# Kernel tuning notes

Measured on AMD Instinct MI355X. Metric: run time of the kernel, lower is better.

## Reference

```python
import jax, jax.numpy as jnp
import numpy as np

B, S, D, H = 2, 2048, 1024, 16
HD = D // H                 # head_dim = 64
BLOCK = 16                  # _DEFAULT_BLOCK_SIZE
NB = S // BLOCK             # max_blocks_per_seq = 128
WINDOW = 512
NEG = jnp.float32(-1e30)


def setup_inputs() -> dict:
    key = jax.random.key(0)
    ks = jax.random.split(key, 5)
    x = jax.random.normal(ks[0], (B, S, D), jnp.float32)
    scale = D ** -0.5
    wq = jax.random.normal(ks[1], (D, D), jnp.float32) * scale
    wk = jax.random.normal(ks[2], (D, D), jnp.float32) * scale
    wv = jax.random.normal(ks[3], (D, D), jnp.float32) * scale
    wo = jax.random.normal(ks[4], (D, D), jnp.float32) * scale
    # sequential paged layout (matches the module's synthesized-cache fallback)
    block_tables = jnp.arange(B * NB, dtype=jnp.int32).reshape(B, NB)
    slot_mapping = jnp.arange(B * S, dtype=jnp.int32)
    context_lens = jnp.full((B,), S, dtype=jnp.int32)
    return {"x": x, "wq": wq, "wk": wk, "wv": wv, "wo": wo,
            "block_tables": block_tables, "slot_mapping": slot_mapping,
            "context_lens": context_lens, "window_size": WINDOW}


def reference(x, wq, wk, wv, wo, block_tables, slot_mapping, context_lens, window_size):
    b, s, d = x.shape
    # Q/K/V projections (nn.Linear, bias=False: y = x @ W^T)
    q = (x @ wq.T).reshape(b, s, H, HD)
    k = (x @ wk.T).reshape(b, s, H, HD)
    v = (x @ wv.T).reshape(b, s, H, HD)

    # ---- memopt_C.write_cache: scatter K/V into the physical slot pool ----
    num_slots = b * s
    key_cache = jnp.zeros((num_slots, H, HD), x.dtype).at[slot_mapping].set(k.reshape(-1, H, HD))
    value_cache = jnp.zeros((num_slots, H, HD), x.dtype).at[slot_mapping].set(v.reshape(-1, H, HD))

    # ---- dynamic_sparse_attention: read KV through block_tables ----
    t = jnp.arange(s)
    # physical slot of logical token t of sequence b: block_tables[b, t//BLOCK]*BLOCK + t%BLOCK
    slots = block_tables[:, t // BLOCK].astype(jnp.int32) * BLOCK + (t % BLOCK)[None, :].astype(jnp.int32)  # [B,S]
    kc = key_cache[slots]    # [B,S,H,HD]
    vc = value_cache[slots]  # [B,S,H,HD]

    scores = jnp.einsum('bqhd,bkhd->bhqk', q, kc) * (HD ** -0.5)  # [B,H,S,S]
    qpos = t[:, None]
    kpos = t[None, :]
    # causal + window-limited visibility (window_size tokens of history)
    vis = (kpos <= qpos) & (qpos - kpos < window_size)            # [S,S]
    ctx = t[None, :] < context_lens[:, None]                       # [B,S]
    mask = vis[None, None, :, :] & ctx[:, None, None, :]
    scores = jnp.where(mask, scores, NEG)
    attn = jax.nn.softmax(scores, axis=-1)
    out = jnp.einsum('bhqk,bkhd->bqhd', attn, vc).reshape(b, s, d)
    return out @ wo.T
```

## Files before the change

kernel.cpp:

```cpp
#include <hip/hip_runtime.h>

typedef __attribute__((ext_vector_type(4))) float  f32x4;
typedef __attribute__((ext_vector_type(8))) short  bf16x8;

typedef __attribute__((address_space(3))) void lds_void_t;
typedef __attribute__((address_space(1))) void g_void_t;

#define S_LEN  2048
#define DMODEL 1024
#define NHEAD  16
#define HDIM   64
#define NBLK   128
#define BATCH  2
#define KT     64
#define VP     72

__device__ __forceinline__ short f2bf(float f) {
  union { float f; unsigned u; } v; v.f = f;
  unsigned r = v.u + 0x7fffu + ((v.u >> 16) & 1u);
  return (short)(r >> 16);
}

__global__ __launch_bounds__(256) void cvt_all_kernel(
    const float* __restrict__ x,  const float* __restrict__ wq,
    const float* __restrict__ wk, const float* __restrict__ wv,
    const float* __restrict__ wo,
    short* __restrict__ xb,  short* __restrict__ wqb,
    short* __restrict__ wkb, short* __restrict__ wvb,
    short* __restrict__ wob) {
  const long i = ((long)blockIdx.x * 256 + threadIdx.x) * 8;
  const float* s; short* d; long off;
  if (i < 4194304L)      { s = x;  d = xb;  off = i; }
  else if (i < 5242880L) { s = wq; d = wqb; off = i - 4194304L; }
  else if (i < 6291456L) { s = wk; d = wkb; off = i - 5242880L; }
  else if (i < 7340032L) { s = wv; d = wvb; off = i - 6291456L; }
  else                   { s = wo; d = wob; off = i - 7340032L; }
  f32x4 a = *(const f32x4*)(s + off);
  f32x4 b = *(const f32x4*)(s + off + 4);
  bf16x8 o;
  o[0]=f2bf(a[0]); o[1]=f2bf(a[1]); o[2]=f2bf(a[2]); o[3]=f2bf(a[3]);
  o[4]=f2bf(b[0]); o[5]=f2bf(b[1]); o[6]=f2bf(b[2]); o[7]=f2bf(b[3]);
  *(bf16x8*)(d + off) = o;
}

__global__ __launch_bounds__(512, 2) void gemm8_kernel(
    const short* __restrict__ A,
    const short* __restrict__ W0, const short* __restrict__ W1, const short* __restrict__ W2,
    const int* __restrict__ slot_map,
    short* __restrict__ qbuf, short* __restrict__ kcache, short* __restrict__ vcache)
{
  extern __shared__ short smem[];

  const int m0 = blockIdx.x * 256;
  const int n0 = blockIdx.y * 192;
  const short* Ag = A + (size_t)m0 * DMODEL;

  const int tid  = threadIdx.x;
  const int wave = tid >> 6, lane = tid & 63;
  const int l15 = lane & 15, lg = lane >> 4;
  const int wr = wave >> 2, wc = wave & 3;
  const int swz = l15 & 7;

  short* const A0s = smem;
  short* const B0s = smem + 16384;
  short* const A1s = smem + 28672;
  short* const B1s = smem + 45056;

  f32x4 acc[8][3];
#pragma unroll
  for (int m = 0; m < 8; m++)
#pragma unroll
    for (int n = 0; n < 3; n++) acc[m][n] = (f32x4)0.f;

#define STAGE_A(DST, K0, P) {                                                              \
    const int gidx = (P) * 512 + tid;                                                      \
    const int r = gidx >> 3;                                                               \
    const int cs = (gidx & 7) ^ (r & 7);                                                   \
    __builtin_amdgcn_global_load_lds((g_void_t*)(Ag + (size_t)r * DMODEL + (K0) + cs * 8), \
        (lds_void_t*)((DST) + ((P) * 512 + wave * 64) * 8), 16, 0, 0); }

#define STAGE_B(DST, K0, P) {                                                              \
    const int gidx = (P) * 512 + tid;                                                      \
    const int r = gidx >> 3;                                                               \
    const int grow = n0 + r;                                                               \
    const short* wb = (grow < 1024) ? W0 : (grow < 2048) ? W1 : W2;                        \
    const int cs = (gidx & 7) ^ (r & 7);                                                   \
    __builtin_amdgcn_global_load_lds((g_void_t*)(wb + (size_t)(grow & 1023) * DMODEL + (K0) + cs * 8), \
        (lds_void_t*)((DST) + ((P) * 512 + wave * 64) * 8), 16, 0, 0); }

#define PHASE_SYNC() do {                                       \
    asm volatile("" ::: "memory");                              \
    __builtin_amdgcn_s_barrier();                               \
    asm volatile("s_waitcnt lgkmcnt(0)" ::: "memory");          \
    __builtin_amdgcn_sched_barrier(0);                          \
  } while (0)

#define PHASE_END() do {                                        \
    asm volatile("" ::: "memory");                              \
    __builtin_amdgcn_s_barrier();                               \
    asm volatile("" ::: "memory");                              \
  } while (0)

#define PHASE_READ_A(BUF, Q)                                                               \
    _Pragma("unroll") for (int mi = 0; mi < 2; ++mi) {                                     \
      const int row = wr * 128 + ((Q) * 2 + mi) * 16 + l15;                                \
      _Pragma("unroll") for (int ks = 0; ks < 2; ++ks)                                     \
        af[mi][ks] = *(const bf16x8*)((BUF) + row * 64 + (((ks * 4 + lg) ^ swz) << 3)); }

#define PHASE_MFMA(Q)                                                                      \
    __builtin_amdgcn_s_setprio(1);                                                         \
    _Pragma("unroll") for (int mi = 0; mi < 2; ++mi)                                       \
    _Pragma("unroll") for (int nt = 0; nt < 3; ++nt)                                       \
    _Pragma("unroll") for (int ks = 0; ks < 2; ++ks)                                       \
      acc[(Q) * 2 + mi][nt] = __builtin_amdgcn_mfma_f32_16x16x32_bf16(                     \
          af[mi][ks], bfr[nt][ks], acc[(Q) * 2 + mi][nt], 0, 0, 0);                        \
    __builtin_amdgcn_s_setprio(0);

  STAGE_B(B0s, 0, 0); STAGE_B(B0s, 0, 1); STAGE_B(B0s, 0, 2);
  STAGE_A(A0s, 0, 0); STAGE_A(A0s, 0, 2); STAGE_A(A0s, 0, 1); STAGE_A(A0s, 0, 3);
  asm volatile("s_waitcnt vmcnt(0)" ::: "memory");
  __builtin_amdgcn_s_barrier();
  asm volatile("" ::: "memory");

  const int NT = DMODEL / 64;
  for (int t = 0; t < NT; ++t) {
    const bool stg = (t + 1 < NT);
    short* const Ac = (t & 1) ? A1s : A0s;
    short* const Bc = (t & 1) ? B1s : B0s;
    short* const An = (t & 1) ? A0s : A1s;
    short* const Bn = (t & 1) ? B0s : B1s;
    const int kn = (t + 1) * 64;

    bf16x8 af[2][2], bfr[3][2];

#pragma unroll
    for (int nt = 0; nt < 3; ++nt) {
      const int row = wc * 48 + nt * 16 + l15;
#pragma unroll
      for (int ks = 0; ks < 2; ++ks)
        bfr[nt][ks] = *(const bf16x8*)(Bc + row * 64 + (((ks * 4 + lg) ^ swz) << 3));
    }
    PHASE_READ_A(Ac, 0);
    if (stg) { STAGE_B(Bn, kn, 0); STAGE_B(Bn, kn, 1); STAGE_B(Bn, kn, 2); }
    PHASE_SYNC();
    PHASE_MFMA(0);
    PHASE_END();

    PHASE_READ_A(Ac, 1);
    if (stg) { STAGE_A(An, kn, 0); STAGE_A(An, kn, 2); }
    PHASE_SYNC();
    PHASE_MFMA(1);
    if (stg) { asm volatile("s_waitcnt vmcnt(6)" ::: "memory"); }
    else     { asm volatile("s_waitcnt vmcnt(1)" ::: "memory"); }
    PHASE_END();

    PHASE_READ_A(Ac, 2);
    if (stg) { STAGE_A(An, kn, 1); }
    PHASE_SYNC();
    PHASE_MFMA(2);
    if (stg) { asm volatile("s_waitcnt vmcnt(6)" ::: "memory"); }
    else     { asm volatile("s_waitcnt vmcnt(0)" ::: "memory"); }
    PHASE_END();

    PHASE_READ_A(Ac, 3);
    if (stg) { STAGE_A(An, kn, 3); }
    PHASE_SYNC();
    PHASE_MFMA(3);
    asm volatile("s_waitcnt vmcnt(2)" ::: "memory");
    PHASE_END();
  }
#undef STAGE_A
#undef STAGE_B
#undef PHASE_SYNC
#undef PHASE_END
#undef PHASE_READ_A
#undef PHASE_MFMA

#pragma unroll
  for (int mf = 0; mf < 8; ++mf) {
    const int rowb = m0 + wr * 128 + mf * 16 + lg * 4;
#pragma unroll
    for (int r4 = 0; r4 < 4; ++r4) {
      const int row = rowb + r4;
      const int slot = slot_map[row];
#pragma unroll
      for (int nt = 0; nt < 3; ++nt) {
        const int col = n0 + wc * 48 + nt * 16 + l15;
        const short bv = f2bf(acc[mf][nt][r4]);
        if (col < DMODEL)
          qbuf[(size_t)row * DMODEL + col] = bv;
        else if (col < 2 * DMODEL)
          kcache[(size_t)slot * DMODEL + (col - DMODEL)] = bv;
        else
          vcache[(size_t)slot * DMODEL + (col - 2 * DMODEL)] = bv;
      }
    }
  }
}

template<int MODE>
__global__ __launch_bounds__(256) void gemm_kernel(
    const short* __restrict__ A,
    const short* __restrict__ W0, const short* __restrict__ W1, const short* __restrict__ W2,
    const int* __restrict__ slot_map,
    short* __restrict__ qbuf, short* __restrict__ kcache, short* __restrict__ vcache,
    float* __restrict__ outf)
{
  __shared__ short As[128 * 32];
  __shared__ short Bs[128 * 32];

  const int m0 = blockIdx.x * 128;
  const int n0 = blockIdx.y * 128;

  const short* Bg;
  if (MODE == 0) {
    const int wsel = n0 >> 10;
    const short* w = (wsel == 0) ? W0 : (wsel == 1) ? W1 : W2;
    Bg = w + (n0 & 1023) * DMODEL;
  } else {
    Bg = W0 + n0 * DMODEL;
  }
  const short* Ag = A + (size_t)m0 * DMODEL;

  const int tid  = threadIdx.x;
  const int wave = tid >> 6, lane = tid & 63;
  const int wr = wave >> 1, wc = wave & 1;
  const int l15 = lane & 15, lg = lane >> 4;

  f32x4 acc[4][4];
#pragma unroll
  for (int m = 0; m < 4; m++)
#pragma unroll
    for (int n = 0; n < 4; n++) acc[m][n] = (f32x4)0.f;

  for (int k0 = 0; k0 < DMODEL; k0 += 32) {
    __syncthreads();
#pragma unroll
    for (int i = 0; i < 2; i++) {
      const int e = i * 256 + tid;
      const int r = e >> 2;
      const int c = (e & 3) << 3;
      const short* ga = Ag + r * DMODEL + k0 + c;
      const short* gb = Bg + r * DMODEL + k0 + c;
      const int ldso = (i * 256 + wave * 64) * 8;
      __builtin_amdgcn_global_load_lds((g_void_t*)(ga), (lds_void_t*)(As + ldso), 16, 0, 0);
      __builtin_amdgcn_global_load_lds((g_void_t*)(gb), (lds_void_t*)(Bs + ldso), 16, 0, 0);
    }
    __syncthreads();

    bf16x8 af[4], bfr[4];
#pragma unroll
    for (int m = 0; m < 4; m++)
      af[m] = *(const bf16x8*)(As + (wr * 64 + m * 16 + l15) * 32 + lg * 8);
#pragma unroll
    for (int n = 0; n < 4; n++)
      bfr[n] = *(const bf16x8*)(Bs + (wc * 64 + n * 16 + l15) * 32 + lg * 8);
#pragma unroll
    for (int m = 0; m < 4; m++)
#pragma unroll
      for (int n = 0; n < 4; n++)
        acc[m][n] = __builtin_amdgcn_mfma_f32_16x16x32_bf16(af[m], bfr[n], acc[m][n], 0, 0, 0);
  }

#pragma unroll
  for (int m = 0; m < 4; m++) {
    const int rowb = m0 + wr * 64 + m * 16 + lg * 4;
#pragma unroll
    for (int n = 0; n < 4; n++) {
      const int col = n0 + wc * 64 + n * 16 + l15;
#pragma unroll
      for (int r = 0; r < 4; r++) {
        const int rw = rowb + r;
        const float val = acc[m][n][r];
        if (MODE == 1) {
          outf[(size_t)rw * DMODEL + col] = val;
        } else {
          const short bv = f2bf(val);
          if (col < DMODEL) {
            qbuf[(size_t)rw * DMODEL + col] = bv;
          } else {
            const int slot = slot_map[rw];
            if (col < 2 * DMODEL)
              kcache[(size_t)slot * DMODEL + (col - DMODEL)] = bv;
            else
              vcache[(size_t)slot * DMODEL + (col - 2 * DMODEL)] = bv;
          }
        }
      }
    }
  }
}

__global__ __launch_bounds__(512, 4) void attn_kernel(
    const short* __restrict__ qbuf,
    const short* __restrict__ kcache, const short* __restrict__ vcache,
    const int* __restrict__ block_tables, const int* __restrict__ context_lens,
    const int* __restrict__ window_size,
    short* __restrict__ attn_out)
{
  __shared__ short Ks[KT * 64];
  __shared__ short Vt[HDIM * VP];
  __shared__ short Pb[8 * 16 * VP];

  const int b = blockIdx.z, h = blockIdx.y, q0 = blockIdx.x * 128;
  const int ctx = context_lens[b];
  const int ws  = window_size[0];
  const int* bt = block_tables + b * NBLK;

  const int tid  = threadIdx.x;
  const int wave = tid >> 6, lane = tid & 63;
  const int l15 = lane & 15, lg = lane >> 4;
  const int qw = q0 + wave * 16;

  const short* qp = qbuf + ((size_t)(b * S_LEN + qw + l15)) * DMODEL + h * HDIM;
  const bf16x8 qf0 = *(const bf16x8*)(qp + lg * 8);
  const bf16x8 qf1 = *(const bf16x8*)(qp + 32 + lg * 8);

  f32x4 oacc[4];
  float lrow[4];
#pragma unroll
  for (int i = 0; i < 4; i++) { oacc[i] = (f32x4)0.f; lrow[i] = 0.f; }

  int kstart = q0 - ws + 1; if (kstart < 0) kstart = 0; kstart &= ~(KT - 1);
  int kend = q0 + 128; if (kend > ctx) kend = ctx;

  const int kr = tid >> 3;
  const int dc = (tid & 7) << 3;
  const float rscale = 0.125f;
  const float FM = 12.f;
  short* pw = Pb + wave * (16 * VP);
  const int swz = (l15 & 7) << 4;

  bf16x8 kreg = (bf16x8)0, vreg = (bf16x8)0;
  {
    const int key = kstart + kr;
    if (key < ctx) {
      const int slot = bt[key >> 4] * 16 + (key & 15);
      kreg = *(const bf16x8*)(kcache + (size_t)slot * DMODEL + h * HDIM + dc);
      vreg = *(const bf16x8*)(vcache + (size_t)slot * DMODEL + h * HDIM + dc);
    }
  }

  for (int kt = kstart; kt < kend; kt += KT) {
    __syncthreads();
    *(bf16x8*)((char*)Ks + kr * 128 + ((dc * 2) ^ ((kr & 7) << 4))) = kreg;
    const int vcol = (kr + dc) & 63;
#pragma unroll
    for (int j = 0; j < 8; j++) Vt[(dc + j) * VP + vcol] = vreg[j];
    kreg = (bf16x8)0; vreg = (bf16x8)0;
    if (kt + KT < kend) {
      const int key = kt + KT + kr;
      if (key < ctx) {
        const int slot = bt[key >> 4] * 16 + (key & 15);
        kreg = *(const bf16x8*)(kcache + (size_t)slot * DMODEL + h * HDIM + dc);
        vreg = *(const bf16x8*)(vcache + (size_t)slot * DMODEL + h * HDIM + dc);
      }
    }
    __syncthreads();

    if ((kt > qw + 15) || (kt + (KT - 1) <= qw - ws)) continue;

    f32x4 sacc[4];
#pragma unroll
    for (int cg = 0; cg < 4; cg++) sacc[cg] = (f32x4)0.f;
#pragma unroll
    for (int cg = 0; cg < 4; cg++) {
      const char* kp = (const char*)Ks + (cg * 16 + l15) * 128;
      const bf16x8 k0 = *(const bf16x8*)(kp + ((lg * 16) ^ swz));
      const bf16x8 k1 = *(const bf16x8*)(kp + ((64 + lg * 16) ^ swz));
      sacc[cg] = __builtin_amdgcn_mfma_f32_16x16x32_bf16(qf0, k0, sacc[cg], 0, 0, 0);
      sacc[cg] = __builtin_amdgcn_mfma_f32_16x16x32_bf16(qf1, k1, sacc[cg], 0, 0, 0);
    }

    const bool fullvis = (kt + (KT - 1) <= qw) && (qw + 15 - kt < ws) && (kt + (KT - 1) < ctx);

    if (fullvis) {
#pragma unroll
      for (int r = 0; r < 4; r++) {
        const float e0 = __expf(sacc[0][r] * rscale - FM);
        const float e1 = __expf(sacc[1][r] * rscale - FM);
        const float e2 = __expf(sacc[2][r] * rscale - FM);
        const float e3 = __expf(sacc[3][r] * rscale - FM);
        lrow[r] += (e0 + e1) + (e2 + e3);
        short* pr = pw + (lg * 4 + r) * VP + l15;
        pr[0]  = f2bf(e0); pr[16] = f2bf(e1);
        pr[32] = f2bf(e2); pr[48] = f2bf(e3);
      }
    } else {
#pragma unroll
      for (int r = 0; r < 4; r++) {
        const int qrow = qw + lg * 4 + r;
        const int key0 = kt + l15;
        const bool ok0 = (key0      <= qrow) && (qrow - key0      < ws) && (key0      < ctx);
        const bool ok1 = (key0 + 16 <= qrow) && (qrow - key0 - 16 < ws) && (key0 + 16 < ctx);
        const bool ok2 = (key0 + 32 <= qrow) && (qrow - key0 - 32 < ws) && (key0 + 32 < ctx);
        const bool ok3 = (key0 + 48 <= qrow) && (qrow - key0 - 48 < ws) && (key0 + 48 < ctx);
        const float e0 = ok0 ? __expf(sacc[0][r] * rscale - FM) : 0.f;
        const float e1 = ok1 ? __expf(sacc[1][r] * rscale - FM) : 0.f;
        const float e2 = ok2 ? __expf(sacc[2][r] * rscale - FM) : 0.f;
        const float e3 = ok3 ? __expf(sacc[3][r] * rscale - FM) : 0.f;
        lrow[r] += (e0 + e1) + (e2 + e3);
        short* pr = pw + (lg * 4 + r) * VP + l15;
        pr[0]  = f2bf(e0); pr[16] = f2bf(e1);
        pr[32] = f2bf(e2); pr[48] = f2bf(e3);
      }
    }

    asm volatile("s_waitcnt lgkmcnt(0)" ::: "memory");

#pragma unroll
    for (int kk = 0; kk < 2; kk++) {
      const bf16x8 pa = *(const bf16x8*)(pw + l15 * VP + kk * 32 + lg * 8);
#pragma unroll
      for (int dn = 0; dn < 4; dn++) {
        const int vrow = dn * 16 + l15;
        const int roff = (kk * 32 + lg * 8 + (vrow & ~7)) & 63;
        const bf16x8 vb = *(const bf16x8*)(Vt + vrow * VP + roff);
        oacc[dn] = __builtin_amdgcn_mfma_f32_16x16x32_bf16(pa, vb, oacc[dn], 0, 0, 0);
      }
    }
  }

#pragma unroll
  for (int r = 0; r < 4; r++) {
    float ls = lrow[r];
    ls += __shfl_xor(ls, 1); ls += __shfl_xor(ls, 2);
    ls += __shfl_xor(ls, 4); ls += __shfl_xor(ls, 8);
    const float inv = 1.f / fmaxf(ls, 1e-30f);
    const int row = qw + lg * 4 + r;
    short* op = attn_out + ((size_t)(b * S_LEN + row)) * DMODEL + h * HDIM;
#pragma unroll
    for (int dn = 0; dn < 4; dn++)
      op[dn * 16 + l15] = f2bf(oacc[dn][r] * inv);
  }
}

extern "C" void kernel_launch(void* const* d_in, const int* in_sizes, int n_in,
                              void* d_out, int out_size, void* d_ws, size_t ws_size,
                              hipStream_t stream) {
  const float* x  = (const float*)d_in[0];
  const float* wq = (const float*)d_in[1];
  const float* wk = (const float*)d_in[2];
  const float* wv = (const float*)d_in[3];
  const float* wo = (const float*)d_in[4];
  const int* block_tables = (const int*)d_in[5];
  const int* slot_mapping = (const int*)d_in[6];
  const int* context_lens = (const int*)d_in[7];
  const int* window_size  = (const int*)d_in[8];
  float* out = (float*)d_out;

  char* ws = (char*)d_ws;
  short* xb     = (short*)(ws + (size_t)( 0 << 20));
  short* wqb    = (short*)(ws + (size_t)( 8 << 20));
  short* wkb    = (short*)(ws + (size_t)(10 << 20));
  short* wvb    = (short*)(ws + (size_t)(12 << 20));
  short* wob    = (short*)(ws + (size_t)(14 << 20));
  short* qbuf   = (short*)(ws + (size_t)(16 << 20));
  short* kcache = (short*)(ws + (size_t)(24 << 20));
  short* vcache = (short*)(ws + (size_t)(32 << 20));
  short* abuf   = (short*)(ws + (size_t)(40 << 20));

  static bool gemm8_init = [] {
    hipFuncSetAttribute(reinterpret_cast<const void*>(&gemm8_kernel),
                        hipFuncAttributeMaxDynamicSharedMemorySize, 114688);
    return true;
  }();
  (void)gemm8_init;

  cvt_all_kernel<<<4096, 256, 0, stream>>>(x, wq, wk, wv, wo, xb, wqb, wkb, wvb, wob);

  gemm8_kernel<<<dim3(16, 16), 512, 114688, stream>>>(xb, wqb, wkb, wvb, slot_mapping,
                                                      qbuf, kcache, vcache);

  attn_kernel<<<dim3(S_LEN / 128, NHEAD, BATCH), 512, 0, stream>>>(
      qbuf, kcache, vcache, block_tables, context_lens, window_size, abuf);

  gemm_kernel<1><<<dim3(32, 8), 256, 0, stream>>>(abuf, wob, nullptr, nullptr, nullptr,
                                                  nullptr, nullptr, nullptr, out);
}
```

Before: 98.95 us.

## Double-buffer output projection GEMM, drop lgkm waits, reverse attention block order

Replaces the output-projection GEMM with a 64x128-tile kernel that uses BK=64, swizzled LDS and double-buffered async global-to-LDS loads, and launches twice as many blocks. This is meant to overlap loads with MFMA and to fill more CUs. The QKV GEMM phases drop the explicit lgkmcnt(0) wait and sched_barrier after the barrier. The attention kernel reverses query-block order for the second batch to balance work across the grid. Removing the lgkm wait relies on the compiler inserting the waits the LDS reads need.

```diff
diff --git a/kernel.cpp b/kernel.cpp
--- a/kernel.cpp
+++ b/kernel.cpp
@@ -88,14 +88,7 @@
     __builtin_amdgcn_global_load_lds((g_void_t*)(wb + (size_t)(grow & 1023) * DMODEL + (K0) + cs * 8), \
         (lds_void_t*)((DST) + ((P) * 512 + wave * 64) * 8), 16, 0, 0); }
 
-#define PHASE_SYNC() do {                                       \
-    asm volatile("" ::: "memory");                              \
-    __builtin_amdgcn_s_barrier();                               \
-    asm volatile("s_waitcnt lgkmcnt(0)" ::: "memory");          \
-    __builtin_amdgcn_sched_barrier(0);                          \
-  } while (0)
-
-#define PHASE_END() do {                                        \
+#define PHASE_BAR() do {                                        \
     asm volatile("" ::: "memory");                              \
     __builtin_amdgcn_s_barrier();                               \
     asm volatile("" ::: "memory");                              \
@@ -142,37 +135,36 @@
     }
     PHASE_READ_A(Ac, 0);
     if (stg) { STAGE_B(Bn, kn, 0); STAGE_B(Bn, kn, 1); STAGE_B(Bn, kn, 2); }
-    PHASE_SYNC();
+    PHASE_BAR();
     PHASE_MFMA(0);
-    PHASE_END();
+    PHASE_BAR();
 
     PHASE_READ_A(Ac, 1);
     if (stg) { STAGE_A(An, kn, 0); STAGE_A(An, kn, 2); }
-    PHASE_SYNC();
+    PHASE_BAR();
     PHASE_MFMA(1);
     if (stg) { asm volatile("s_waitcnt vmcnt(6)" ::: "memory"); }
     else     { asm volatile("s_waitcnt vmcnt(1)" ::: "memory"); }
-    PHASE_END();
+    PHASE_BAR();
 
     PHASE_READ_A(Ac, 2);
     if (stg) { STAGE_A(An, kn, 1); }
-    PHASE_SYNC();
+    PHASE_BAR();
     PHASE_MFMA(2);
     if (stg) { asm volatile("s_waitcnt vmcnt(6)" ::: "memory"); }
     else     { asm volatile("s_waitcnt vmcnt(0)" ::: "memory"); }
-    PHASE_END();
+    PHASE_BAR();
 
     PHASE_READ_A(Ac, 3);
     if (stg) { STAGE_A(An, kn, 3); }
-    PHASE_SYNC();
+    PHASE_BAR();
     PHASE_MFMA(3);
     asm volatile("s_waitcnt vmcnt(2)" ::: "memory");
-    PHASE_END();
+    PHASE_BAR();
   }
 #undef STAGE_A
 #undef STAGE_B
-#undef PHASE_SYNC
-#undef PHASE_END
+#undef PHASE_BAR
 #undef PHASE_READ_A
 #undef PHASE_MFMA
 
@@ -198,95 +190,96 @@
   }
 }
 
-template<int MODE>
-__global__ __launch_bounds__(256) void gemm_kernel(
-    const short* __restrict__ A,
-    const short* __restrict__ W0, const short* __restrict__ W1, const short* __restrict__ W2,
-    const int* __restrict__ slot_map,
-    short* __restrict__ qbuf, short* __restrict__ kcache, short* __restrict__ vcache,
+__global__ __launch_bounds__(256) void gemm1_kernel(
+    const short* __restrict__ A, const short* __restrict__ W,
     float* __restrict__ outf)
 {
-  __shared__ short As[128 * 32];
-  __shared__ short Bs[128 * 32];
-
-  const int m0 = blockIdx.x * 128;
+  __shared__ short As[2][64 * 64];
+  __shared__ short Bs[2][128 * 64];
+
+  const int m0 = blockIdx.x * 64;
   const int n0 = blockIdx.y * 128;
-
-  const short* Bg;
-  if (MODE == 0) {
-    const int wsel = n0 >> 10;
-    const short* w = (wsel == 0) ? W0 : (wsel == 1) ? W1 : W2;
-    Bg = w + (n0 & 1023) * DMODEL;
-  } else {
-    Bg = W0 + n0 * DMODEL;
-  }
   const short* Ag = A + (size_t)m0 * DMODEL;
-
-  const int tid  = threadIdx.x;
+  const short* Bg = W + (size_t)n0 * DMODEL;
+
+  const int tid = threadIdx.x;
   const int wave = tid >> 6, lane = tid & 63;
-  const int wr = wave >> 1, wc = wave & 1;
   const int l15 = lane & 15, lg = lane >> 4;
-
-  f32x4 acc[4][4];
+  const int swz = l15 & 7;
+
+  f32x4 acc[4][2];
 #pragma unroll
   for (int m = 0; m < 4; m++)
 #pragma unroll
-    for (int n = 0; n < 4; n++) acc[m][n] = (f32x4)0.f;
-
-  for (int k0 = 0; k0 < DMODEL; k0 += 32) {
-    __syncthreads();
-#pragma unroll
-    for (int i = 0; i < 2; i++) {
-      const int e = i * 256 + tid;
-      const int r = e >> 2;
-      const int c = (e & 3) << 3;
-      const short* ga = Ag + r * DMODEL + k0 + c;
-      const short* gb = Bg + r * DMODEL + k0 + c;
-      const int ldso = (i * 256 + wave * 64) * 8;
-      __builtin_amdgcn_global_load_lds((g_void_t*)(ga), (lds_void_t*)(As + ldso), 16, 0, 0);
-      __builtin_amdgcn_global_load_lds((g_void_t*)(gb), (lds_void_t*)(Bs + ldso), 16, 0, 0);
-    }
-    __syncthreads();
-
-    bf16x8 af[4], bfr[4];
-#pragma unroll
-    for (int m = 0; m < 4; m++)
-      af[m] = *(const bf16x8*)(As + (wr * 64 + m * 16 + l15) * 32 + lg * 8);
-#pragma unroll
-    for (int n = 0; n < 4; n++)
-      bfr[n] = *(const bf16x8*)(Bs + (wc * 64 + n * 16 + l15) * 32 + lg * 8);
-#pragma unroll
-    for (int m = 0; m < 4; m++)
-#pragma unroll
-      for (int n = 0; n < 4; n++)
-        acc[m][n] = __builtin_amdgcn_mfma_f32_16x16x32_bf16(af[m], bfr[n], acc[m][n], 0, 0, 0);
-  }
-
-#pragma unroll
-  for (int m = 0; m < 4; m++) {
-    const int rowb = m0 + wr * 64 + m * 16 + lg * 4;
-#pragma unroll
-    for (int n = 0; n < 4; n++) {
-      const int col = n0 + wc * 64 + n * 16 + l15;
-#pragma unroll
-      for (int r = 0; r < 4; r++) {
-        const int rw = rowb + r;
-        const float val = acc[m][n][r];
-        if (MODE == 1) {
-          outf[(size_t)rw * DMODEL + col] = val;
-        } else {
-          const short bv = f2bf(val);
-          if (col < DMODEL) {
-            qbuf[(size_t)rw * DMODEL + col] = bv;
-          } else {
-            const int slot = slot_map[rw];
-            if (col < 2 * DMODEL)
-              kcache[(size_t)slot * DMODEL + (col - DMODEL)] = bv;
-            else
-              vcache[(size_t)slot * DMODEL + (col - 2 * DMODEL)] = bv;
-          }
-        }
-      }
+    for (int n = 0; n < 2; n++) acc[m][n] = (f32x4)0.f;
+
+#define STG1(BUF, K0) {                                                                    \
+    _Pragma("unroll") for (int p = 0; p < 2; ++p) {                                        \
+      const int u = p * 256 + tid; const int r = u >> 3; const int cs = (u & 7) ^ (r & 7); \
+      __builtin_amdgcn_global_load_lds((g_void_t*)(Ag + (size_t)r * DMODEL + (K0) + cs * 8), \
+          (lds_void_t*)(As[BUF] + (p * 256 + wave * 64) * 8), 16, 0, 0); }                 \
+    _Pragma("unroll") for (int p = 0; p < 4; ++p) {                                        \
+      const int u = p * 256 + tid; const int r = u >> 3; const int cs = (u & 7) ^ (r & 7); \
+      __builtin_amdgcn_global_load_lds((g_void_t*)(Bg + (size_t)r * DMODEL + (K0) + cs * 8), \
+          (lds_void_t*)(Bs[BUF] + (p * 256 + wave * 64) * 8), 16, 0, 0); } }
+
+  STG1(0, 0);
+  asm volatile("s_waitcnt vmcnt(0)" ::: "memory");
+  __builtin_amdgcn_s_barrier();
+  asm volatile("" ::: "memory");
+
+  for (int t = 0; t < 16; ++t) {
+    const int cur = t & 1;
+    if (t + 1 < 16) {
+      STG1(cur ^ 1, (t + 1) * 64);
+      asm volatile("s_waitcnt vmcnt(6)" ::: "memory");
+    } else {
+      asm volatile("s_waitcnt vmcnt(0)" ::: "memory");
+    }
+    asm volatile("" ::: "memory");
+    __builtin_amdgcn_s_barrier();
+    asm volatile("" ::: "memory");
+
+    bf16x8 af[4][2], bfr[2][2];
+#pragma unroll
+    for (int m4 = 0; m4 < 4; ++m4) {
+      const int row = m4 * 16 + l15;
+#pragma unroll
+      for (int ks = 0; ks < 2; ++ks)
+        af[m4][ks] = *(const bf16x8*)(As[cur] + row * 64 + (((ks * 4 + lg) ^ swz) << 3));
+    }
+#pragma unroll
+    for (int n2 = 0; n2 < 2; ++n2) {
+      const int row = wave * 32 + n2 * 16 + l15;
+#pragma unroll
+      for (int ks = 0; ks < 2; ++ks)
+        bfr[n2][ks] = *(const bf16x8*)(Bs[cur] + row * 64 + (((ks * 4 + lg) ^ swz) << 3));
+    }
+    __builtin_amdgcn_s_setprio(1);
+#pragma unroll
+    for (int m4 = 0; m4 < 4; ++m4)
+#pragma unroll
+      for (int n2 = 0; n2 < 2; ++n2)
+#pragma unroll
+        for (int ks = 0; ks < 2; ++ks)
+          acc[m4][n2] = __builtin_amdgcn_mfma_f32_16x16x32_bf16(af[m4][ks], bfr[n2][ks], acc[m4][n2], 0, 0, 0);
+    __builtin_amdgcn_s_setprio(0);
+
+    asm volatile("" ::: "memory");
+    __builtin_amdgcn_s_barrier();
+    asm volatile("" ::: "memory");
+  }
+#undef STG1
+
+#pragma unroll
+  for (int m4 = 0; m4 < 4; ++m4) {
+    const int rowb = m0 + m4 * 16 + lg * 4;
+#pragma unroll
+    for (int n2 = 0; n2 < 2; ++n2) {
+      const int col = n0 + wave * 32 + n2 * 16 + l15;
+#pragma unroll
+      for (int r4 = 0; r4 < 4; ++r4)
+        outf[(size_t)(rowb + r4) * DMODEL + col] = acc[m4][n2][r4];
     }
   }
 }
@@ -302,7 +295,9 @@
   __shared__ short Vt[HDIM * VP];
   __shared__ short Pb[8 * 16 * VP];
 
-  const int b = blockIdx.z, h = blockIdx.y, q0 = blockIdx.x * 128;
+  const int b = blockIdx.z, h = blockIdx.y;
+  const int bx = (b & 1) ? ((int)gridDim.x - 1 - (int)blockIdx.x) : (int)blockIdx.x;
+  const int q0 = bx * 128;
   const int ctx = context_lens[b];
   const int ws  = window_size[0];
   const int* bt = block_tables + b * NBLK;
@@ -475,6 +470,5 @@
   attn_kernel<<<dim3(S_LEN / 128, NHEAD, BATCH), 512, 0, stream>>>(
       qbuf, kcache, vcache, block_tables, context_lens, window_size, abuf);
 
-  gemm_kernel<1><<<dim3(32, 8), 256, 0, stream>>>(abuf, wob, nullptr, nullptr, nullptr,
-                                                  nullptr, nullptr, nullptr, out);
-}
+  gemm1_kernel<<<dim3(64, 8), 256, 0, stream>>>(abuf, wob, out);
+}
```

Result: faster. 90.61 us (-8.4%).
